# Performance work log

Hardware: AMD Instinct MI355X
Metric: run time of the kernel (lower is better)

## Reference

```python
import jax, jax.numpy as jnp
import numpy as np
import math

HIDDEN = 2048
N_Q = 16
N_KV = 8
HEAD_DIM = 128
THETA = 10000.0
RANK = 8
ALPHA = 16
LORA_SCALING = ALPHA / RANK  # 2.0
SCALING = 1.0 / math.sqrt(HEAD_DIM)


def setup_inputs() -> dict:
    key = jax.random.key(0)
    ks = jax.random.split(key, 14)
    B, S = 2, 2048
    std = 0.02
    inp = {
        "x": jax.random.normal(ks[0], (B, S, HIDDEN), dtype=jnp.float32),
        # nn.Linear weights: [out_features, in_features]
        "Wq": jax.random.normal(ks[1], (N_Q * HEAD_DIM, HIDDEN), dtype=jnp.float32) * std,
        "Wk": jax.random.normal(ks[2], (N_KV * HEAD_DIM, HIDDEN), dtype=jnp.float32) * std,
        "Wv": jax.random.normal(ks[3], (N_KV * HEAD_DIM, HIDDEN), dtype=jnp.float32) * std,
        "Wo": jax.random.normal(ks[4], (HIDDEN, N_Q * HEAD_DIM), dtype=jnp.float32) * std,
        "qA": jax.random.normal(ks[5], (RANK, HIDDEN), dtype=jnp.float32) * std,
        "qB": jax.random.normal(ks[6], (N_Q * HEAD_DIM, RANK), dtype=jnp.float32) * std,
        "kA": jax.random.normal(ks[7], (RANK, HIDDEN), dtype=jnp.float32) * std,
        "kB": jax.random.normal(ks[8], (N_KV * HEAD_DIM, RANK), dtype=jnp.float32) * std,
        "vA": jax.random.normal(ks[9], (RANK, HIDDEN), dtype=jnp.float32) * std,
        "vB": jax.random.normal(ks[10], (N_KV * HEAD_DIM, RANK), dtype=jnp.float32) * std,
        "oA": jax.random.normal(ks[11], (RANK, N_Q * HEAD_DIM), dtype=jnp.float32) * std,
        "oB": jax.random.normal(ks[12], (HIDDEN, RANK), dtype=jnp.float32) * std,
    }
    return inp


def _rope_cos_sin(seq_len, dtype):
    inv_freq = 1.0 / (THETA ** (jnp.arange(0, HEAD_DIM, 2, dtype=jnp.float32) / HEAD_DIM))
    t = jnp.arange(seq_len, dtype=jnp.float32)
    freqs = t[:, None] * inv_freq[None, :]  # [S, D/2]
    return jnp.cos(freqs).astype(dtype), jnp.sin(freqs).astype(dtype)


def _apply_rope(x, cos, sin):
    # x: [B, H, S, D]; interleaved real/imag pairs on last dim
    xr = x[..., ::2]
    xi = x[..., 1::2]
    rr = xr * cos - xi * sin
    ri = xr * sin + xi * cos
    return jnp.stack([rr, ri], axis=-1).reshape(x.shape)


def _forward(x, Wq, Wk, Wv, Wo, qA, qB, kA, kB, vA, vB, oA, oB):
    B, S, H = x.shape
    # base projections + LoRA (low-rank path kept factored: (x @ A^T) @ B^T)
    q = x @ Wq.T + ((x @ qA.T) @ qB.T) * LORA_SCALING  # [B,S,NQ*D]
    k = x @ Wk.T + ((x @ kA.T) @ kB.T) * LORA_SCALING  # [B,S,NKV*D]
    v = x @ Wv.T + ((x @ vA.T) @ vB.T) * LORA_SCALING
    q = q.reshape(B, S, N_Q, HEAD_DIM).transpose(0, 2, 1, 3)   # [B,NQ,S,D]
    k = k.reshape(B, S, N_KV, HEAD_DIM).transpose(0, 2, 1, 3)  # [B,NKV,S,D]
    v = v.reshape(B, S, N_KV, HEAD_DIM).transpose(0, 2, 1, 3)
    cos, sin = _rope_cos_sin(S, x.dtype)  # [S, D/2] each
    q = _apply_rope(q, cos, sin)
    k = _apply_rope(k, cos, sin)
    if N_Q != N_KV:
        rep = N_Q // N_KV
        k = jnp.repeat(k, rep, axis=1)  # [B,NQ,S,D]
        v = jnp.repeat(v, rep, axis=1)
    scores = jnp.einsum('bhqd,bhkd->bhqk', q, k) * SCALING
    causal = jnp.tril(jnp.ones((S, S), dtype=bool))
    scores = jnp.where(causal, scores, -jnp.inf)
    attn = jax.nn.softmax(scores, axis=-1).astype(v.dtype)
    out = jnp.einsum('bhqk,bhkd->bhqd', attn, v)  # [B,NQ,S,D]
    out = out.transpose(0, 2, 1, 3).reshape(B, S, N_Q * HEAD_DIM)
    return out @ Wo.T + ((out @ oA.T) @ oB.T) * LORA_SCALING


def reference(x, Wq, Wk, Wv, Wo, qA, qB, kA, kB, vA, vB, oA, oB):
    return _forward(x, Wq, Wk, Wv, Wo, qA, qB, kA, kB, vA, vB, oA, oB)
```

## Files before the change

### kernel.cpp

```cpp
#include <hip/hip_runtime.h>
#include <hip/hip_bf16.h>
#include <cmath>

#define HIDDEN 2048
#define SEQ 2048
#define BATCH 2
#define NQ 16
#define NKV 8
#define HD 128
#define RANKL 8
#define LORA_SCALE 2.0f
#define INV_SQRT_D 0.08838834764831845f
#define LOG2E 1.4426950408889634f
#define SM_SCALE (INV_SQRT_D * LOG2E)

typedef unsigned short ushort_t;
typedef __bf16 bf16x8 __attribute__((ext_vector_type(8)));
typedef float f32x4 __attribute__((ext_vector_type(4)));

static __device__ __forceinline__ ushort_t f2bf(float f) {
    __hip_bfloat16 h = __float2bfloat16(f);
    return *(ushort_t*)&h;
}
static __device__ __forceinline__ float bf2f(ushort_t u) {
    unsigned int v = ((unsigned int)u) << 16;
    return __builtin_bit_cast(float, v);
}
static __device__ __forceinline__ void gload_lds16(const ushort_t* g, ushort_t* l) {
    __builtin_amdgcn_global_load_lds(
        (const __attribute__((address_space(1))) unsigned int*)g,
        (__attribute__((address_space(3))) unsigned int*)l, 16, 0, 0);
}

__global__ __launch_bounds__(256) void lora_cast_x(
    const float* __restrict__ X, ushort_t* __restrict__ Xbf,
    const float* __restrict__ qA, const float* __restrict__ kA,
    const float* __restrict__ vA,
    float* __restrict__ oq, float* __restrict__ ok, float* __restrict__ ov)
{
    int m = blockIdx.x;
    int t = threadIdx.x;
    int c0 = t * 8;
    const float* xr = X + (size_t)m * HIDDEN + c0;
    float4 a = *(const float4*)xr;
    float4 b = *(const float4*)(xr + 4);
    float xv[8] = {a.x, a.y, a.z, a.w, b.x, b.y, b.z, b.w};
    uint4 o;
    o.x = (unsigned int)f2bf(xv[0]) | ((unsigned int)f2bf(xv[1]) << 16);
    o.y = (unsigned int)f2bf(xv[2]) | ((unsigned int)f2bf(xv[3]) << 16);
    o.z = (unsigned int)f2bf(xv[4]) | ((unsigned int)f2bf(xv[5]) << 16);
    o.w = (unsigned int)f2bf(xv[6]) | ((unsigned int)f2bf(xv[7]) << 16);
    *(uint4*)(Xbf + (size_t)m * HIDDEN + c0) = o;

    float p[3][RANKL];
#pragma unroll
    for (int w = 0; w < 3; w++)
#pragma unroll
        for (int r = 0; r < RANKL; r++) p[w][r] = 0.f;
    const float* Aw[3] = {qA, kA, vA};
#pragma unroll
    for (int e = 0; e < 8; e++) {
        float x8 = xv[e];
#pragma unroll
        for (int w = 0; w < 3; w++)
#pragma unroll
            for (int r = 0; r < RANKL; r++)
                p[w][r] += x8 * Aw[w][r * HIDDEN + c0 + e];
    }
#pragma unroll
    for (int w = 0; w < 3; w++)
#pragma unroll
        for (int r = 0; r < RANKL; r++) {
            float v = p[w][r];
            v += __shfl_xor(v, 32); v += __shfl_xor(v, 16);
            v += __shfl_xor(v, 8);  v += __shfl_xor(v, 4);
            v += __shfl_xor(v, 2);  v += __shfl_xor(v, 1);
            p[w][r] = v;
        }
    __shared__ float wred[4][3][RANKL];
    int wave = t >> 6, lane = t & 63;
    if (lane == 0) {
#pragma unroll
        for (int w = 0; w < 3; w++)
#pragma unroll
            for (int r = 0; r < RANKL; r++) wred[wave][w][r] = p[w][r];
    }
    __syncthreads();
    if (t < 3 * RANKL) {
        int w = t / RANKL, r = t % RANKL;
        float s = wred[0][w][r] + wred[1][w][r] + wred[2][w][r] + wred[3][w][r];
        float* dst = (w == 0) ? oq : (w == 1) ? ok : ov;
        dst[(size_t)m * RANKL + r] = s;
    }
}

__global__ __launch_bounds__(256) void lora_xa_bf16(
    const ushort_t* __restrict__ X, const float* __restrict__ Aw,
    float* __restrict__ out, int K)
{
    int m = blockIdx.x;
    int t = threadIdx.x;
    const ushort_t* xr = X + (size_t)m * K;
    float p[RANKL];
#pragma unroll
    for (int r = 0; r < RANKL; r++) p[r] = 0.f;
    for (int c = t; c < K; c += 256) {
        float xv = bf2f(xr[c]);
#pragma unroll
        for (int r = 0; r < RANKL; r++) p[r] += xv * Aw[r * K + c];
    }
#pragma unroll
    for (int r = 0; r < RANKL; r++) {
        float v = p[r];
        v += __shfl_xor(v, 32); v += __shfl_xor(v, 16);
        v += __shfl_xor(v, 8);  v += __shfl_xor(v, 4);
        v += __shfl_xor(v, 2);  v += __shfl_xor(v, 1);
        p[r] = v;
    }
    __shared__ float wred[4][RANKL];
    int wave = t >> 6, lane = t & 63;
    if (lane == 0) {
#pragma unroll
        for (int r = 0; r < RANKL; r++) wred[wave][r] = p[r];
    }
    __syncthreads();
    if (t < RANKL) {
        out[(size_t)m * RANKL + t] =
            wred[0][t] + wred[1][t] + wred[2][t] + wred[3][t];
    }
}

__global__ __launch_bounds__(256) void cast_weights(
    const float* __restrict__ Wq, const float* __restrict__ Wk,
    const float* __restrict__ Wv, const float* __restrict__ Wo,
    ushort_t* __restrict__ Wqb, ushort_t* __restrict__ Wkb,
    ushort_t* __restrict__ Wvb, ushort_t* __restrict__ Wob)
{
    size_t i = (size_t)blockIdx.x * 256 + threadIdx.x;
    const float* src; ushort_t* dst; size_t j;
    if (i < 524288)       { src = Wq; dst = Wqb; j = i; }
    else if (i < 786432)  { src = Wk; dst = Wkb; j = i - 524288; }
    else if (i < 1048576) { src = Wv; dst = Wvb; j = i - 786432; }
    else                  { src = Wo; dst = Wob; j = i - 1048576; }
    const float4* p = (const float4*)src + j * 2;
    float4 a = p[0], b = p[1];
    uint4 o;
    o.x = (unsigned int)f2bf(a.x) | ((unsigned int)f2bf(a.y) << 16);
    o.y = (unsigned int)f2bf(a.z) | ((unsigned int)f2bf(a.w) << 16);
    o.z = (unsigned int)f2bf(b.x) | ((unsigned int)f2bf(b.y) << 16);
    o.w = (unsigned int)f2bf(b.z) | ((unsigned int)f2bf(b.w) << 16);
    *(uint4*)(dst + j * 8) = o;
}

static __device__ __forceinline__ void gemm_core(
    const ushort_t* __restrict__ A, const ushort_t* __restrict__ B,
    void* __restrict__ Cout, int N, int K, int bm, int bn,
    const float* __restrict__ xa, const float* __restrict__ LB,
    float lscale, int out_bf16, ushort_t* As, ushort_t* Bs)
{
    const int t = threadIdx.x;
    const int lane = t & 63;
    const int w = t >> 6;
    const int quad = lane >> 4;
    const int c = lane & 15;

    const int wm = (w & 1) * 64;
    const int wn = (w >> 1) * 64;

    f32x4 acc[4][4];
#pragma unroll
    for (int i = 0; i < 4; i++)
#pragma unroll
        for (int j = 0; j < 4; j++) acc[i][j] = (f32x4){0.f, 0.f, 0.f, 0.f};

    const int p0 = w * 64 + lane;
    const int p1 = 256 + w * 64 + lane;
    const int r0 = p0 >> 2, g0 = (p0 & 3) ^ ((p0 >> 3) & 3);
    const int r1 = p1 >> 2, g1 = (p1 & 3) ^ ((p1 >> 3) & 3);
    const ushort_t* gA0 = A + (size_t)(bm + r0) * K + g0 * 8;
    const ushort_t* gA1 = A + (size_t)(bm + r1) * K + g1 * 8;
    const ushort_t* gB0 = B + (size_t)(bn + r0) * K + g0 * 8;
    const ushort_t* gB1 = B + (size_t)(bn + r1) * K + g1 * 8;
    ushort_t* lA0 = As + (size_t)(w * 64) * 8;
    ushort_t* lA1 = As + (size_t)(256 + w * 64) * 8;
    ushort_t* lB0 = Bs + (size_t)(w * 64) * 8;
    ushort_t* lB1 = Bs + (size_t)(256 + w * 64) * 8;

    const int csw = quad ^ ((c >> 1) & 3);

    for (int k0 = 0; k0 < K; k0 += 32) {
        __syncthreads();
        gload_lds16(gA0 + k0, lA0);
        gload_lds16(gA1 + k0, lA1);
        gload_lds16(gB0 + k0, lB0);
        gload_lds16(gB1 + k0, lB1);
        __syncthreads();

        bf16x8 af[4], bfr[4];
#pragma unroll
        for (int mt = 0; mt < 4; mt++)
            af[mt] = *(const bf16x8*)&As[((wm + mt * 16 + c) * 4 + csw) * 8];
#pragma unroll
        for (int nt = 0; nt < 4; nt++)
            bfr[nt] = *(const bf16x8*)&Bs[((wn + nt * 16 + c) * 4 + csw) * 8];
#pragma unroll
        for (int mt = 0; mt < 4; mt++)
#pragma unroll
            for (int nt = 0; nt < 4; nt++)
                acc[mt][nt] = __builtin_amdgcn_mfma_f32_16x16x32_bf16(
                    af[mt], bfr[nt], acc[mt][nt], 0, 0, 0);
    }

    float lb[4][RANKL];
#pragma unroll
    for (int nt = 0; nt < 4; nt++) {
        int col = bn + wn + nt * 16 + c;
        float4 u = *(const float4*)&LB[(size_t)col * RANKL];
        float4 v = *(const float4*)&LB[(size_t)col * RANKL + 4];
        lb[nt][0] = u.x; lb[nt][1] = u.y; lb[nt][2] = u.z; lb[nt][3] = u.w;
        lb[nt][4] = v.x; lb[nt][5] = v.y; lb[nt][6] = v.z; lb[nt][7] = v.w;
    }
#pragma unroll
    for (int mt = 0; mt < 4; mt++) {
        float la[4][RANKL];
#pragma unroll
        for (int r = 0; r < 4; r++) {
            int row = bm + wm + mt * 16 + quad * 4 + r;
            float4 u = *(const float4*)&xa[(size_t)row * RANKL];
            float4 v = *(const float4*)&xa[(size_t)row * RANKL + 4];
            la[r][0] = u.x; la[r][1] = u.y; la[r][2] = u.z; la[r][3] = u.w;
            la[r][4] = v.x; la[r][5] = v.y; la[r][6] = v.z; la[r][7] = v.w;
        }
#pragma unroll
        for (int nt = 0; nt < 4; nt++) {
#pragma unroll
            for (int r = 0; r < 4; r++) {
                float s = 0.f;
#pragma unroll
                for (int k = 0; k < RANKL; k++) s += la[r][k] * lb[nt][k];
                float val = acc[mt][nt][r] + lscale * s;
                size_t row = bm + wm + mt * 16 + quad * 4 + r;
                size_t col = bn + wn + nt * 16 + c;
                if (out_bf16)
                    ((ushort_t*)Cout)[row * N + col] = f2bf(val);
                else
                    ((float*)Cout)[row * N + col] = val;
            }
        }
    }
}

__global__ __launch_bounds__(256) void gemm_qkv(
    const ushort_t* __restrict__ A,
    const ushort_t* __restrict__ Wqb, const ushort_t* __restrict__ Wkb,
    const ushort_t* __restrict__ Wvb,
    ushort_t* __restrict__ q_lin, ushort_t* __restrict__ k_lin,
    ushort_t* __restrict__ v_lin,
    const float* __restrict__ xa_q, const float* __restrict__ xa_k,
    const float* __restrict__ xa_v,
    const float* __restrict__ qB, const float* __restrict__ kB,
    const float* __restrict__ vB)
{
    __shared__ ushort_t As[128 * 32];
    __shared__ ushort_t Bs[128 * 32];
    int bc = blockIdx.y;
    const ushort_t* B; ushort_t* Cout; const float* xa; const float* LB;
    int N, bn;
    if (bc < 16)      { B = Wqb; Cout = q_lin; xa = xa_q; LB = qB; N = 2048; bn = bc * 128; }
    else if (bc < 24) { B = Wkb; Cout = k_lin; xa = xa_k; LB = kB; N = 1024; bn = (bc - 16) * 128; }
    else              { B = Wvb; Cout = v_lin; xa = xa_v; LB = vB; N = 1024; bn = (bc - 24) * 128; }
    gemm_core(A, B, Cout, N, HIDDEN, blockIdx.x * 128, bn, xa, LB,
              LORA_SCALE, 1, As, Bs);
}

__global__ __launch_bounds__(256) void gemm_wo(
    const ushort_t* __restrict__ A, const ushort_t* __restrict__ Wob,
    float* __restrict__ out, const float* __restrict__ xa_o,
    const float* __restrict__ oB)
{
    __shared__ ushort_t As[128 * 32];
    __shared__ ushort_t Bs[128 * 32];
    gemm_core(A, Wob, out, HIDDEN, NQ * HD, blockIdx.x * 128, blockIdx.y * 128,
              xa_o, oB, LORA_SCALE, 0, As, Bs);
}

__global__ __launch_bounds__(256) void rope_qk(
    const ushort_t* __restrict__ qlin, const ushort_t* __restrict__ klin,
    ushort_t* __restrict__ qb, ushort_t* __restrict__ kb)
{
    int bs = blockIdx.x;
    int s = bs & (SEQ - 1);
    int b = bs >> 11;
    int t = threadIdx.x;
    int p = t & 63;
    float inv = exp2f(-(float)p * 0.20762050593046f);
    float ang = (float)s * inv;
    float cc = cosf(ang), si = sinf(ang);
#pragma unroll
    for (int j = 0; j < 6; j++) {
        int item = t + 256 * j;
        int hh = item >> 6;
        unsigned int pk;
        ushort_t* dst;
        if (hh < NQ) {
            pk = *(const unsigned int*)&qlin[(size_t)bs * (NQ * HD) + hh * HD + 2 * p];
            dst = qb + (((size_t)(b * NQ + hh) * SEQ) + s) * HD + 2 * p;
        } else {
            int kh = hh - NQ;
            pk = *(const unsigned int*)&klin[(size_t)bs * (NKV * HD) + kh * HD + 2 * p];
            dst = kb + (((size_t)(b * NKV + kh) * SEQ) + s) * HD + 2 * p;
        }
        float xr = bf2f((ushort_t)(pk & 0xffff));
        float xi = bf2f((ushort_t)(pk >> 16));
        float rr = xr * cc - xi * si;
        float ri = xr * si + xi * cc;
        *(unsigned int*)dst = ((unsigned int)f2bf(ri) << 16) | f2bf(rr);
    }
}

__global__ __launch_bounds__(256) void v_transpose(
    const ushort_t* __restrict__ vlin, ushort_t* __restrict__ Vt)
{
    int bk = blockIdx.x;
    int b = bk >> 3, kvh = bk & 7;
    int s0 = blockIdx.y * 64, d0 = blockIdx.z * 64;
    __shared__ ushort_t tile[64 * 72];
    int t = threadIdx.x;
#pragma unroll
    for (int i = 0; i < 2; i++) {
        int id = t + 256 * i;
        int r = id >> 3, cc = id & 7;
        uint4 v = *(const uint4*)&vlin[(size_t)(b * SEQ + s0 + r) * (NKV * HD)
                                       + kvh * HD + d0 + cc * 8];
        *(uint4*)&tile[r * 72 + cc * 8] = v;
    }
    __syncthreads();
#pragma unroll
    for (int i = 0; i < 2; i++) {
        int id = t + 256 * i;
        int dr = id >> 3, sc = id & 7;
        ushort_t tmp[8];
#pragma unroll
        for (int e = 0; e < 8; e++) tmp[e] = tile[(sc * 8 + e) * 72 + dr];
        *(uint4*)&Vt[((size_t)(b * NKV + kvh) * HD + d0 + dr) * SEQ + s0 + sc * 8]
            = *(uint4*)tmp;
    }
}

__global__ __launch_bounds__(256, 2) void attn_mfma3(
    const ushort_t* __restrict__ Q, const ushort_t* __restrict__ K,
    const ushort_t* __restrict__ V, ushort_t* __restrict__ O)
{
    __shared__ ushort_t Ks[2][64 * 128];
    __shared__ ushort_t Vs[2][128 * 64];
    __shared__ ushort_t Psh[4][16 * 68];

    const int t = threadIdx.x;
    const int lane = t & 63;
    const int w = t >> 6;
    const int quad = lane >> 4;
    const int c = lane & 15;
    const int q4 = quad * 4;
    const int c7 = c & 7;

    const int head = blockIdx.x >> 4;
    const int a = blockIdx.x & 15;
    const int h = head & (NQ - 1);
    const int b = head >> 4;
    const int kvh = b * NKV + (h >> 1);

    const ushort_t* Kg = K + (size_t)kvh * SEQ * HD;
    const ushort_t* Vg = V + (size_t)kvh * HD * SEQ;

    const ushort_t* gK[4]; const ushort_t* gV[4];
    int lo[4];
#pragma unroll
    for (int i = 0; i < 4; i++) {
        int cid = t + 256 * i;
        int kr = cid >> 4, kc = cid & 15;
        gK[i] = Kg + (size_t)kr * HD + ((kc ^ (kr & 7)) * 8);
        int vd = cid >> 3, vc = cid & 7;
        gV[i] = Vg + (size_t)vd * SEQ + ((vc ^ (vd & 7)) * 8);
        lo[i] = (i * 256 + (t & ~63)) * 8;
    }

#pragma unroll 1
    for (int half = 0; half < 2; half++) {
        const int qt = half ? (31 - a) : a;
        const int qb0 = qt * 64;
        const int myrow = qb0 + w * 16;

        const ushort_t* Qg = Q + ((size_t)head * SEQ + myrow + c) * HD;
        bf16x8 qf[4];
#pragma unroll
        for (int ch = 0; ch < 4; ch++)
            qf[ch] = *(const bf16x8*)(Qg + ch * 32 + quad * 8);

        f32x4 o[8];
#pragma unroll
        for (int i = 0; i < 8; i++) o[i] = (f32x4){0.f, 0.f, 0.f, 0.f};
        float lp[4] = {0.f, 0.f, 0.f, 0.f};

        const int ntiles = qt + 1;

#pragma unroll
        for (int i = 0; i < 4; i++) gload_lds16(gK[i], &Ks[0][lo[i]]);
#pragma unroll
        for (int i = 0; i < 4; i++) gload_lds16(gV[i], &Vs[0][lo[i]]);
        __syncthreads();

        for (int tile = 0; tile < ntiles; ++tile) {
            const int cur = tile & 1;
            if (tile + 1 < ntiles) {
                const int j1 = (tile + 1) * 64;
#pragma unroll
                for (int i = 0; i < 4; i++)
                    gload_lds16(gK[i] + (size_t)j1 * HD, &Ks[cur ^ 1][lo[i]]);
#pragma unroll
                for (int i = 0; i < 4; i++)
                    gload_lds16(gV[i] + j1, &Vs[cur ^ 1][lo[i]]);
            }

            f32x4 s[4];
#pragma unroll
            for (int tt = 0; tt < 4; tt++) s[tt] = (f32x4){0.f, 0.f, 0.f, 0.f};
#pragma unroll
            for (int tt = 0; tt < 4; tt++) {
                const int krow = tt * 16 + c;
#pragma unroll
                for (int ch = 0; ch < 4; ch++) {
                    bf16x8 kf = *(const bf16x8*)
                        &Ks[cur][krow * 128 + (((ch * 4 + quad) ^ c7) * 8)];
                    s[tt] = __builtin_amdgcn_mfma_f32_16x16x32_bf16(
                        qf[ch], kf, s[tt], 0, 0, 0);
                }
            }

            const bool diag = (tile == qt);
            const int j0 = tile * 64;
#pragma unroll
            for (int r = 0; r < 4; r++) {
                const int row_g = myrow + q4 + r;
#pragma unroll
                for (int tt = 0; tt < 4; tt++) {
                    float p = exp2f(s[tt][r] * SM_SCALE);
                    if (diag && (j0 + tt * 16 + c > row_g)) p = 0.f;
                    Psh[w][(q4 + r) * 68 + tt * 16 + c] = f2bf(p);
                    lp[r] += p;
                }
            }

            bf16x8 pf[2];
#pragma unroll
            for (int ch = 0; ch < 2; ch++) {
                int base = c * 68 + ch * 32 + quad * 8;
                uint2 aa = *(const uint2*)&Psh[w][base];
                uint2 bb = *(const uint2*)&Psh[w][base + 4];
                uint4 u; u.x = aa.x; u.y = aa.y; u.z = bb.x; u.w = bb.y;
                pf[ch] = __builtin_bit_cast(bf16x8, u);
            }

#pragma unroll
            for (int dt = 0; dt < 8; dt++) {
                const int vrow = dt * 16 + c;
#pragma unroll
                for (int ch = 0; ch < 2; ch++) {
                    bf16x8 vf = *(const bf16x8*)
                        &Vs[cur][vrow * 64 + (((ch * 4 + quad) ^ c7) * 8)];
                    o[dt] = __builtin_amdgcn_mfma_f32_16x16x32_bf16(
                        pf[ch], vf, o[dt], 0, 0, 0);
                }
            }
            __syncthreads();
        }

        float inv[4];
#pragma unroll
        for (int r = 0; r < 4; r++) {
            float v = lp[r];
            v += __shfl_xor(v, 1);
            v += __shfl_xor(v, 2);
            v += __shfl_xor(v, 4);
            v += __shfl_xor(v, 8);
            inv[r] = 1.f / v;
        }
        size_t base = ((size_t)b * SEQ + myrow + q4) * (NQ * HD) + h * HD + c;
#pragma unroll
        for (int r = 0; r < 4; r++)
#pragma unroll
            for (int dt = 0; dt < 8; dt++)
                O[base + (size_t)r * (NQ * HD) + dt * 16] =
                    f2bf(o[dt][r] * inv[r]);
    }
}

extern "C" void kernel_launch(void* const* d_in, const int* in_sizes, int n_in,
                              void* d_out, int out_size, void* d_ws, size_t ws_size,
                              hipStream_t stream)
{
    const float* x  = (const float*)d_in[0];
    const float* Wq = (const float*)d_in[1];
    const float* Wk = (const float*)d_in[2];
    const float* Wv = (const float*)d_in[3];
    const float* Wo = (const float*)d_in[4];
    const float* qA = (const float*)d_in[5];
    const float* qB = (const float*)d_in[6];
    const float* kA = (const float*)d_in[7];
    const float* kB = (const float*)d_in[8];
    const float* vA = (const float*)d_in[9];
    const float* vB = (const float*)d_in[10];
    const float* oA = (const float*)d_in[11];
    const float* oB = (const float*)d_in[12];
    float* out = (float*)d_out;
    float* ws = (float*)d_ws;

    const int M = BATCH * SEQ;

    float* xa_q = ws;
    float* xa_k = ws + 32768;
    float* xa_v = ws + 65536;
    float* xa_o = ws + 98304;
    ushort_t* q_lin = (ushort_t*)(ws + 131072);
    ushort_t* k_lin = (ushort_t*)(ws + 4325376);
    ushort_t* v_lin = (ushort_t*)(ws + 6422528);
    ushort_t* qb    = (ushort_t*)(ws + 8519680);
    ushort_t* kb    = (ushort_t*)(ws + 12713984);
    ushort_t* vtb   = (ushort_t*)(ws + 14811136);
    ushort_t* xbf   = (ushort_t*)(ws + 16908288);
    ushort_t* Wqb   = (ushort_t*)(ws + 21102592);
    ushort_t* Wkb   = (ushort_t*)(ws + 23199744);
    ushort_t* Wvb   = (ushort_t*)(ws + 24248320);
    ushort_t* Wob   = (ushort_t*)(ws + 25296896);
    ushort_t* attn_out = q_lin;

    lora_cast_x<<<M, 256, 0, stream>>>(x, xbf, qA, kA, vA, xa_q, xa_k, xa_v);

    cast_weights<<<6144, 256, 0, stream>>>(Wq, Wk, Wv, Wo, Wqb, Wkb, Wvb, Wob);

    gemm_qkv<<<dim3(M / 128, 32), 256, 0, stream>>>(
        xbf, Wqb, Wkb, Wvb, q_lin, k_lin, v_lin,
        xa_q, xa_k, xa_v, qB, kB, vB);

    rope_qk<<<M, 256, 0, stream>>>(q_lin, k_lin, qb, kb);
    v_transpose<<<dim3(BATCH * NKV, SEQ / 64, HD / 64), 256, 0, stream>>>(v_lin, vtb);

    attn_mfma3<<<512, 256, 0, stream>>>(qb, kb, vtb, attn_out);

    lora_xa_bf16<<<M, 256, 0, stream>>>(attn_out, oA, xa_o, NQ * HD);
    gemm_wo<<<dim3(M / 128, HIDDEN / 128), 256, 0, stream>>>(
        attn_out, Wob, out, xa_o, oB);
}
```

Baseline: 419.9 us.

## Fuse prep and rope/transpose kernels; restructure attention to 128-row query tiles

```diff
diff --git a/kernel.cpp b/kernel.cpp
--- a/kernel.cpp
+++ b/kernel.cpp
@@ -32,14 +32,39 @@
         (__attribute__((address_space(3))) unsigned int*)l, 16, 0, 0);
 }
 
-__global__ __launch_bounds__(256) void lora_cast_x(
+__global__ __launch_bounds__(256) void prep_kernel(
     const float* __restrict__ X, ushort_t* __restrict__ Xbf,
     const float* __restrict__ qA, const float* __restrict__ kA,
     const float* __restrict__ vA,
-    float* __restrict__ oq, float* __restrict__ ok, float* __restrict__ ov)
-{
-    int m = blockIdx.x;
-    int t = threadIdx.x;
+    float* __restrict__ oq, float* __restrict__ ok, float* __restrict__ ov,
+    const float* __restrict__ Wq, const float* __restrict__ Wk,
+    const float* __restrict__ Wv, const float* __restrict__ Wo,
+    ushort_t* __restrict__ Wqb, ushort_t* __restrict__ Wkb,
+    ushort_t* __restrict__ Wvb, ushort_t* __restrict__ Wob)
+{
+    __shared__ float wred[4][3][RANKL];
+    const int blk = blockIdx.x;
+    const int t = threadIdx.x;
+
+    if (blk >= 4096) {
+        size_t i = (size_t)(blk - 4096) * 256 + t;
+        const float* src; ushort_t* dst; size_t j;
+        if (i < 524288)       { src = Wq; dst = Wqb; j = i; }
+        else if (i < 786432)  { src = Wk; dst = Wkb; j = i - 524288; }
+        else if (i < 1048576) { src = Wv; dst = Wvb; j = i - 786432; }
+        else                  { src = Wo; dst = Wob; j = i - 1048576; }
+        const float4* p = (const float4*)src + j * 2;
+        float4 a = p[0], b = p[1];
+        uint4 o;
+        o.x = (unsigned int)f2bf(a.x) | ((unsigned int)f2bf(a.y) << 16);
+        o.y = (unsigned int)f2bf(a.z) | ((unsigned int)f2bf(a.w) << 16);
+        o.z = (unsigned int)f2bf(b.x) | ((unsigned int)f2bf(b.y) << 16);
+        o.w = (unsigned int)f2bf(b.z) | ((unsigned int)f2bf(b.w) << 16);
+        *(uint4*)(dst + j * 8) = o;
+        return;
+    }
+
+    int m = blk;
     int c0 = t * 8;
     const float* xr = X + (size_t)m * HIDDEN + c0;
     float4 a = *(const float4*)xr;
@@ -77,7 +102,6 @@
             v += __shfl_xor(v, 2);  v += __shfl_xor(v, 1);
             p[w][r] = v;
         }
-    __shared__ float wred[4][3][RANKL];
     int wave = t >> 6, lane = t & 63;
     if (lane == 0) {
 #pragma unroll
@@ -128,28 +152,6 @@
         out[(size_t)m * RANKL + t] =
             wred[0][t] + wred[1][t] + wred[2][t] + wred[3][t];
     }
-}
-
-__global__ __launch_bounds__(256) void cast_weights(
-    const float* __restrict__ Wq, const float* __restrict__ Wk,
-    const float* __restrict__ Wv, const float* __restrict__ Wo,
-    ushort_t* __restrict__ Wqb, ushort_t* __restrict__ Wkb,
-    ushort_t* __restrict__ Wvb, ushort_t* __restrict__ Wob)
-{
-    size_t i = (size_t)blockIdx.x * 256 + threadIdx.x;
-    const float* src; ushort_t* dst; size_t j;
-    if (i < 524288)       { src = Wq; dst = Wqb; j = i; }
-    else if (i < 786432)  { src = Wk; dst = Wkb; j = i - 524288; }
-    else if (i < 1048576) { src = Wv; dst = Wvb; j = i - 786432; }
-    else                  { src = Wo; dst = Wob; j = i - 1048576; }
-    const float4* p = (const float4*)src + j * 2;
-    float4 a = p[0], b = p[1];
-    uint4 o;
-    o.x = (unsigned int)f2bf(a.x) | ((unsigned int)f2bf(a.y) << 16);
-    o.y = (unsigned int)f2bf(a.z) | ((unsigned int)f2bf(a.w) << 16);
-    o.z = (unsigned int)f2bf(b.x) | ((unsigned int)f2bf(b.y) << 16);
-    o.w = (unsigned int)f2bf(b.z) | ((unsigned int)f2bf(b.w) << 16);
-    *(uint4*)(dst + j * 8) = o;
 }
 
 static __device__ __forceinline__ void gemm_core(
@@ -284,52 +286,55 @@
               xa_o, oB, LORA_SCALE, 0, As, Bs);
 }
 
-__global__ __launch_bounds__(256) void rope_qk(
+__global__ __launch_bounds__(256) void rope_vt(
     const ushort_t* __restrict__ qlin, const ushort_t* __restrict__ klin,
-    ushort_t* __restrict__ qb, ushort_t* __restrict__ kb)
-{
-    int bs = blockIdx.x;
-    int s = bs & (SEQ - 1);
-    int b = bs >> 11;
-    int t = threadIdx.x;
-    int p = t & 63;
-    float inv = exp2f(-(float)p * 0.20762050593046f);
-    float ang = (float)s * inv;
-    float cc = cosf(ang), si = sinf(ang);
-#pragma unroll
-    for (int j = 0; j < 6; j++) {
-        int item = t + 256 * j;
-        int hh = item >> 6;
-        unsigned int pk;
-        ushort_t* dst;
-        if (hh < NQ) {
-            pk = *(const unsigned int*)&qlin[(size_t)bs * (NQ * HD) + hh * HD + 2 * p];
-            dst = qb + (((size_t)(b * NQ + hh) * SEQ) + s) * HD + 2 * p;
-        } else {
-            int kh = hh - NQ;
-            pk = *(const unsigned int*)&klin[(size_t)bs * (NKV * HD) + kh * HD + 2 * p];
-            dst = kb + (((size_t)(b * NKV + kh) * SEQ) + s) * HD + 2 * p;
-        }
-        float xr = bf2f((ushort_t)(pk & 0xffff));
-        float xi = bf2f((ushort_t)(pk >> 16));
-        float rr = xr * cc - xi * si;
-        float ri = xr * si + xi * cc;
-        *(unsigned int*)dst = ((unsigned int)f2bf(ri) << 16) | f2bf(rr);
-    }
-}
-
-__global__ __launch_bounds__(256) void v_transpose(
-    const ushort_t* __restrict__ vlin, ushort_t* __restrict__ Vt)
-{
-    int bk = blockIdx.x;
+    const ushort_t* __restrict__ vlin,
+    ushort_t* __restrict__ qb, ushort_t* __restrict__ kb,
+    ushort_t* __restrict__ vtb)
+{
+    __shared__ ushort_t tile[64 * 72];
+    const int t = threadIdx.x;
+
+    if (blockIdx.x < 4096) {
+        int bs = blockIdx.x;
+        int s = bs & (SEQ - 1);
+        int b = bs >> 11;
+        int p = t & 63;
+        float inv = exp2f(-(float)p * 0.20762050593046f);
+        float ang = (float)s * inv;
+        float cc = cosf(ang), si = sinf(ang);
+#pragma unroll
+        for (int j = 0; j < 6; j++) {
+            int item = t + 256 * j;
+            int hh = item >> 6;
+            unsigned int pk;
+            ushort_t* dst;
+            if (hh < NQ) {
+                pk = *(const unsigned int*)&qlin[(size_t)bs * (NQ * HD) + hh * HD + 2 * p];
+                dst = qb + (((size_t)(b * NQ + hh) * SEQ) + s) * HD + 2 * p;
+            } else {
+                int kh = hh - NQ;
+                pk = *(const unsigned int*)&klin[(size_t)bs * (NKV * HD) + kh * HD + 2 * p];
+                dst = kb + (((size_t)(b * NKV + kh) * SEQ) + s) * HD + 2 * p;
+            }
+            float xr = bf2f((ushort_t)(pk & 0xffff));
+            float xi = bf2f((ushort_t)(pk >> 16));
+            float rr = xr * cc - xi * si;
+            float ri = xr * si + xi * cc;
+            *(unsigned int*)dst = ((unsigned int)f2bf(ri) << 16) | f2bf(rr);
+        }
+        return;
+    }
+
+    int id = blockIdx.x - 4096;
+    int bk = id & 15;
     int b = bk >> 3, kvh = bk & 7;
-    int s0 = blockIdx.y * 64, d0 = blockIdx.z * 64;
-    __shared__ ushort_t tile[64 * 72];
-    int t = threadIdx.x;
+    int s0 = ((id >> 4) & 31) * 64;
+    int d0 = (id >> 9) * 64;
 #pragma unroll
     for (int i = 0; i < 2; i++) {
-        int id = t + 256 * i;
-        int r = id >> 3, cc = id & 7;
+        int e = t + 256 * i;
+        int r = e >> 3, cc = e & 7;
         uint4 v = *(const uint4*)&vlin[(size_t)(b * SEQ + s0 + r) * (NKV * HD)
                                        + kvh * HD + d0 + cc * 8];
         *(uint4*)&tile[r * 72 + cc * 8] = v;
@@ -337,23 +342,23 @@
     __syncthreads();
 #pragma unroll
     for (int i = 0; i < 2; i++) {
-        int id = t + 256 * i;
-        int dr = id >> 3, sc = id & 7;
+        int e = t + 256 * i;
+        int dr = e >> 3, sc = e & 7;
         ushort_t tmp[8];
 #pragma unroll
-        for (int e = 0; e < 8; e++) tmp[e] = tile[(sc * 8 + e) * 72 + dr];
-        *(uint4*)&Vt[((size_t)(b * NKV + kvh) * HD + d0 + dr) * SEQ + s0 + sc * 8]
+        for (int j = 0; j < 8; j++) tmp[j] = tile[(sc * 8 + j) * 72 + dr];
+        *(uint4*)&vtb[((size_t)(b * NKV + kvh) * HD + d0 + dr) * SEQ + s0 + sc * 8]
             = *(uint4*)tmp;
     }
 }
 
-__global__ __launch_bounds__(256, 2) void attn_mfma3(
+__global__ __launch_bounds__(256) void attn_mfma7(
     const ushort_t* __restrict__ Q, const ushort_t* __restrict__ K,
     const ushort_t* __restrict__ V, ushort_t* __restrict__ O)
 {
-    __shared__ ushort_t Ks[2][64 * 128];
-    __shared__ ushort_t Vs[2][128 * 64];
-    __shared__ ushort_t Psh[4][16 * 68];
+    __shared__ ushort_t Ks[64 * 128];
+    __shared__ ushort_t Vs[128 * 64];
+    __shared__ ushort_t Psh[4][2][16 * 68];
 
     const int t = threadIdx.x;
     const int lane = t & 63;
@@ -363,8 +368,8 @@
     const int q4 = quad * 4;
     const int c7 = c & 7;
 
-    const int head = blockIdx.x >> 4;
-    const int a = blockIdx.x & 15;
+    const int qb = 15 - (blockIdx.x >> 5);
+    const int head = blockIdx.x & 31;
     const int h = head & (NQ - 1);
     const int b = head >> 4;
     const int kvh = b * NKV + (h >> 1);
@@ -373,7 +378,7 @@
     const ushort_t* Vg = V + (size_t)kvh * HD * SEQ;
 
     const ushort_t* gK[4]; const ushort_t* gV[4];
-    int lo[4];
+    int lo4[4];
 #pragma unroll
     for (int i = 0; i < 4; i++) {
         int cid = t + 256 * i;
@@ -381,116 +386,125 @@
         gK[i] = Kg + (size_t)kr * HD + ((kc ^ (kr & 7)) * 8);
         int vd = cid >> 3, vc = cid & 7;
         gV[i] = Vg + (size_t)vd * SEQ + ((vc ^ (vd & 7)) * 8);
-        lo[i] = (i * 256 + (t & ~63)) * 8;
-    }
-
-#pragma unroll 1
-    for (int half = 0; half < 2; half++) {
-        const int qt = half ? (31 - a) : a;
-        const int qb0 = qt * 64;
-        const int myrow = qb0 + w * 16;
-
-        const ushort_t* Qg = Q + ((size_t)head * SEQ + myrow + c) * HD;
-        bf16x8 qf[4];
+        lo4[i] = (i * 256 + (t & ~63)) * 8;
+    }
+
+    bf16x8 qf[2][4];
+#pragma unroll
+    for (int mt = 0; mt < 2; mt++) {
+        const ushort_t* Qg = Q +
+            ((size_t)head * SEQ + qb * 128 + w * 32 + mt * 16 + c) * HD;
 #pragma unroll
         for (int ch = 0; ch < 4; ch++)
-            qf[ch] = *(const bf16x8*)(Qg + ch * 32 + quad * 8);
-
-        f32x4 o[8];
-#pragma unroll
-        for (int i = 0; i < 8; i++) o[i] = (f32x4){0.f, 0.f, 0.f, 0.f};
-        float lp[4] = {0.f, 0.f, 0.f, 0.f};
-
-        const int ntiles = qt + 1;
-
-#pragma unroll
-        for (int i = 0; i < 4; i++) gload_lds16(gK[i], &Ks[0][lo[i]]);
-#pragma unroll
-        for (int i = 0; i < 4; i++) gload_lds16(gV[i], &Vs[0][lo[i]]);
+            qf[mt][ch] = *(const bf16x8*)(Qg + ch * 32 + quad * 8);
+    }
+
+    f32x4 o[2][8];
+#pragma unroll
+    for (int mt = 0; mt < 2; mt++)
+#pragma unroll
+        for (int i = 0; i < 8; i++) o[mt][i] = (f32x4){0.f, 0.f, 0.f, 0.f};
+    float lp[2][4] = {{0.f, 0.f, 0.f, 0.f}, {0.f, 0.f, 0.f, 0.f}};
+
+    const int ntiles = 2 * qb + 2;
+    const int mask_from = 2 * qb;
+
+    for (int tile = 0; tile < ntiles; ++tile) {
+        const int j0 = tile * 64;
         __syncthreads();
-
-        for (int tile = 0; tile < ntiles; ++tile) {
-            const int cur = tile & 1;
-            if (tile + 1 < ntiles) {
-                const int j1 = (tile + 1) * 64;
-#pragma unroll
-                for (int i = 0; i < 4; i++)
-                    gload_lds16(gK[i] + (size_t)j1 * HD, &Ks[cur ^ 1][lo[i]]);
-#pragma unroll
-                for (int i = 0; i < 4; i++)
-                    gload_lds16(gV[i] + j1, &Vs[cur ^ 1][lo[i]]);
+#pragma unroll
+        for (int i = 0; i < 4; i++)
+            gload_lds16(gK[i] + (size_t)j0 * HD, &Ks[lo4[i]]);
+#pragma unroll
+        for (int i = 0; i < 4; i++)
+            gload_lds16(gV[i] + j0, &Vs[lo4[i]]);
+        __syncthreads();
+
+        f32x4 s[2][4];
+#pragma unroll
+        for (int tt = 0; tt < 4; tt++) {
+            s[0][tt] = (f32x4){0.f, 0.f, 0.f, 0.f};
+            s[1][tt] = (f32x4){0.f, 0.f, 0.f, 0.f};
+        }
+#pragma unroll
+        for (int tt = 0; tt < 4; tt++) {
+            const int krow = tt * 16 + c;
+#pragma unroll
+            for (int ch = 0; ch < 4; ch++) {
+                bf16x8 kf = *(const bf16x8*)
+                    &Ks[krow * 128 + (((ch * 4 + quad) ^ c7) * 8)];
+                s[0][tt] = __builtin_amdgcn_mfma_f32_16x16x32_bf16(
+                    qf[0][ch], kf, s[0][tt], 0, 0, 0);
+                s[1][tt] = __builtin_amdgcn_mfma_f32_16x16x32_bf16(
+                    qf[1][ch], kf, s[1][tt], 0, 0, 0);
             }
-
-            f32x4 s[4];
-#pragma unroll
-            for (int tt = 0; tt < 4; tt++) s[tt] = (f32x4){0.f, 0.f, 0.f, 0.f};
-#pragma unroll
-            for (int tt = 0; tt < 4; tt++) {
-                const int krow = tt * 16 + c;
-#pragma unroll
-                for (int ch = 0; ch < 4; ch++) {
-                    bf16x8 kf = *(const bf16x8*)
-                        &Ks[cur][krow * 128 + (((ch * 4 + quad) ^ c7) * 8)];
-                    s[tt] = __builtin_amdgcn_mfma_f32_16x16x32_bf16(
-                        qf[ch], kf, s[tt], 0, 0, 0);
+        }
+
+        const bool need_mask = (tile >= mask_from);
+#pragma unroll
+        for (int mt = 0; mt < 2; mt++) {
+            ushort_t* Pw = Psh[w][mt];
+            const int rowbase = qb * 128 + w * 32 + mt * 16;
+#pragma unroll
+            for (int r = 0; r < 4; r++) {
+                const int row_g = rowbase + q4 + r;
+#pragma unroll
+                for (int tt = 0; tt < 4; tt++) {
+                    float p = exp2f(s[mt][tt][r] * SM_SCALE);
+                    if (need_mask && (j0 + tt * 16 + c > row_g)) p = 0.f;
+                    Pw[(q4 + r) * 68 + tt * 16 + c] = f2bf(p);
+                    lp[mt][r] += p;
                 }
             }
-
-            const bool diag = (tile == qt);
-            const int j0 = tile * 64;
-#pragma unroll
-            for (int r = 0; r < 4; r++) {
-                const int row_g = myrow + q4 + r;
-#pragma unroll
-                for (int tt = 0; tt < 4; tt++) {
-                    float p = exp2f(s[tt][r] * SM_SCALE);
-                    if (diag && (j0 + tt * 16 + c > row_g)) p = 0.f;
-                    Psh[w][(q4 + r) * 68 + tt * 16 + c] = f2bf(p);
-                    lp[r] += p;
-                }
-            }
-
-            bf16x8 pf[2];
+        }
+
+        bf16x8 pf[2][2];
+#pragma unroll
+        for (int mt = 0; mt < 2; mt++)
 #pragma unroll
             for (int ch = 0; ch < 2; ch++) {
                 int base = c * 68 + ch * 32 + quad * 8;
-                uint2 aa = *(const uint2*)&Psh[w][base];
-                uint2 bb = *(const uint2*)&Psh[w][base + 4];
+                uint2 aa = *(const uint2*)&Psh[w][mt][base];
+                uint2 bb = *(const uint2*)&Psh[w][mt][base + 4];
                 uint4 u; u.x = aa.x; u.y = aa.y; u.z = bb.x; u.w = bb.y;
-                pf[ch] = __builtin_bit_cast(bf16x8, u);
+                pf[mt][ch] = __builtin_bit_cast(bf16x8, u);
             }
 
 #pragma unroll
-            for (int dt = 0; dt < 8; dt++) {
-                const int vrow = dt * 16 + c;
-#pragma unroll
-                for (int ch = 0; ch < 2; ch++) {
-                    bf16x8 vf = *(const bf16x8*)
-                        &Vs[cur][vrow * 64 + (((ch * 4 + quad) ^ c7) * 8)];
-                    o[dt] = __builtin_amdgcn_mfma_f32_16x16x32_bf16(
-                        pf[ch], vf, o[dt], 0, 0, 0);
-                }
+        for (int dt = 0; dt < 8; dt++) {
+            const int vrow = dt * 16 + c;
+#pragma unroll
+            for (int ch = 0; ch < 2; ch++) {
+                bf16x8 vf = *(const bf16x8*)
+                    &Vs[vrow * 64 + (((ch * 4 + quad) ^ c7) * 8)];
+                o[0][dt] = __builtin_amdgcn_mfma_f32_16x16x32_bf16(
+                    pf[0][ch], vf, o[0][dt], 0, 0, 0);
+                o[1][dt] = __builtin_amdgcn_mfma_f32_16x16x32_bf16(
+                    pf[1][ch], vf, o[1][dt], 0, 0, 0);
             }
-            __syncthreads();
-        }
-
+        }
+    }
+
+#pragma unroll
+    for (int mt = 0; mt < 2; mt++) {
         float inv[4];
 #pragma unroll
         for (int r = 0; r < 4; r++) {
-            float v = lp[r];
+            float v = lp[mt][r];
             v += __shfl_xor(v, 1);
             v += __shfl_xor(v, 2);
             v += __shfl_xor(v, 4);
             v += __shfl_xor(v, 8);
             inv[r] = 1.f / v;
         }
-        size_t base = ((size_t)b * SEQ + myrow + q4) * (NQ * HD) + h * HD + c;
+        size_t base = ((size_t)b * SEQ + qb * 128 + w * 32 + mt * 16 + q4)
+                      * (NQ * HD) + h * HD + c;
 #pragma unroll
         for (int r = 0; r < 4; r++)
 #pragma unroll
             for (int dt = 0; dt < 8; dt++)
                 O[base + (size_t)r * (NQ * HD) + dt * 16] =
-                    f2bf(o[dt][r] * inv[r]);
+                    f2bf(o[mt][dt][r] * inv[r]);
     }
 }
 
@@ -526,25 +540,24 @@
     ushort_t* qb    = (ushort_t*)(ws + 8519680);
     ushort_t* kb    = (ushort_t*)(ws + 12713984);
     ushort_t* vtb   = (ushort_t*)(ws + 14811136);
-    ushort_t* xbf   = (ushort_t*)(ws + 16908288);
-    ushort_t* Wqb   = (ushort_t*)(ws + 21102592);
-    ushort_t* Wkb   = (ushort_t*)(ws + 23199744);
-    ushort_t* Wvb   = (ushort_t*)(ws + 24248320);
-    ushort_t* Wob   = (ushort_t*)(ws + 25296896);
-    ushort_t* attn_out = q_lin;
-
-    lora_cast_x<<<M, 256, 0, stream>>>(x, xbf, qA, kA, vA, xa_q, xa_k, xa_v);
-
-    cast_weights<<<6144, 256, 0, stream>>>(Wq, Wk, Wv, Wo, Wqb, Wkb, Wvb, Wob);
+    ushort_t* attn_out = (ushort_t*)(ws + 16908288);
+    ushort_t* xbf   = (ushort_t*)(ws + 21102592);
+    ushort_t* Wqb   = (ushort_t*)(ws + 25296896);
+    ushort_t* Wkb   = (ushort_t*)(ws + 27394048);
+    ushort_t* Wvb   = (ushort_t*)(ws + 28442624);
+    ushort_t* Wob   = (ushort_t*)(ws + 29491200);
+
+    prep_kernel<<<10240, 256, 0, stream>>>(
+        x, xbf, qA, kA, vA, xa_q, xa_k, xa_v,
+        Wq, Wk, Wv, Wo, Wqb, Wkb, Wvb, Wob);
 
     gemm_qkv<<<dim3(M / 128, 32), 256, 0, stream>>>(
         xbf, Wqb, Wkb, Wvb, q_lin, k_lin, v_lin,
         xa_q, xa_k, xa_v, qB, kB, vB);
 
-    rope_qk<<<M, 256, 0, stream>>>(q_lin, k_lin, qb, kb);
-    v_transpose<<<dim3(BATCH * NKV, SEQ / 64, HD / 64), 256, 0, stream>>>(v_lin, vtb);
-
-    attn_mfma3<<<512, 256, 0, stream>>>(qb, kb, vtb, attn_out);
+    rope_vt<<<5120, 256, 0, stream>>>(q_lin, k_lin, v_lin, qb, kb, vtb);
+
+    attn_mfma7<<<512, 256, 0, stream>>>(qb, kb, vtb, attn_out);
 
     lora_xa_bf16<<<M, 256, 0, stream>>>(attn_out, oA, xa_o, NQ * HD);
     gemm_wo<<<dim3(M / 128, HIDDEN / 128), 256, 0, stream>>>(
```

Result: slower. 448.9 us (+6.9%).
